# Kernel tuning notes

Measured on AMD Instinct MI355X. Metric: run time of the kernel, lower is better.

The kernel has to match this reference:

```python
import jax, jax.numpy as jnp
import numpy as np

# ---- config (matches init_kwargs) ----
B, C_IN, L, T = 32, 12, 1024, 64
C1, C2, K = 64, 128, 7
PAD = K // 2
NUM_CLASSES = 4
GAIN = 2.0
TH1, TH2 = 0.5, 0.5
TAU1, TAU2 = 1.0, 0.9
RESET = 0.0


def setup_inputs() -> dict:
    key = jax.random.key(0)
    ks = jax.random.split(key, 7)
    x = jax.random.normal(ks[0], (B, C_IN, L, T), dtype=jnp.float32)
    w1 = jax.random.normal(ks[1], (C1, C_IN, K), dtype=jnp.float32) * 0.1
    b1 = jax.random.normal(ks[2], (C1,), dtype=jnp.float32) * 0.01
    w2 = jax.random.normal(ks[3], (C2, C1, K), dtype=jnp.float32) * 0.05
    b2 = jax.random.normal(ks[4], (C2,), dtype=jnp.float32) * 0.01
    fc_w = jax.random.normal(ks[5], (NUM_CLASSES, C2), dtype=jnp.float32) * 0.1
    fc_b = jax.random.normal(ks[6], (NUM_CLASSES,), dtype=jnp.float32) * 0.01
    return {"x": x, "w1": w1, "b1": b1, "w2": w2, "b2": b2, "fc_w": fc_w, "fc_b": fc_b}


def _conv1d(x, w, b):
    # x: [B, Cin, L], w: [Cout, Cin, K] -> [B, Cout, L] (same padding)
    y = jax.lax.conv_general_dilated(
        x, w, window_strides=(1,), padding=[(PAD, PAD)],
        dimension_numbers=("NCW", "OIW", "NCW"))
    return y + b[None, :, None]


def _lif(v, inp, tau, thresh):
    # v <- v + (inp - v)/tau; spike = (v >= thresh); reset spiked neurons
    v = v + (inp - v) / tau
    spike = (v >= thresh).astype(inp.dtype)
    v = jnp.where(spike > 0, jnp.asarray(RESET, inp.dtype), v)
    return v, spike


def reference(x, w1, b1, w2, b2, fc_w, fc_b):
    # QuantStub/DeQuantStub are identity in the fp32 eager model.
    xs = jnp.transpose(x, (3, 0, 1, 2))  # [T, B, C_IN, L]

    def step(carry, xt):
        v1, v2, acc = carry
        h1 = _conv1d(xt, w1, b1) * GAIN
        v1, s1 = _lif(v1, h1, TAU1, TH1)
        h2 = _conv1d(s1, w2, b2) * GAIN
        v2, s2 = _lif(v2, h2, TAU2, TH2)
        return (v1, v2, acc + s2), None

    v1_0 = jnp.zeros((B, C1, L), x.dtype)
    v2_0 = jnp.zeros((B, C2, L), x.dtype)
    acc0 = jnp.zeros((B, C2, L), x.dtype)
    (_, _, acc), _ = jax.lax.scan(step, (v1_0, v2_0, acc0), xs)

    out = acc / jnp.asarray(T, x.dtype)          # [B, C2, L]
    out = jnp.mean(out, axis=-1)                  # AdaptiveAvgPool1d(1) + squeeze
    return out @ fc_w.T + fc_b                    # [B, NUM_CLASSES]
```

## Files before the change

### kernel.cpp

```cpp
#include <hip/hip_runtime.h>
#include <hip/hip_bf16.h>
#include <cstdint>

#define B_   32
#define CIN  12
#define L_   1024
#define T_   64
#define C1_  64
#define C2_  128
#define K_   7
#define PAD_ 3

typedef __attribute__((ext_vector_type(8))) short short8;
typedef __attribute__((ext_vector_type(4))) float float4v;

#define WS_S1T   0ull
#define WS_W2HI  268435456ull
#define WS_W1F   (WS_W2HI + 114688ull)
#define WS_POOL  (WS_W1F + 32768ull)
#define WS_ZP    (WS_POOL + 16384ull)

#define GLOAD_LDS(SRC, DST)                                                        \
    __builtin_amdgcn_global_load_lds(                                              \
        (const __attribute__((address_space(1))) unsigned int*)(const void*)(SRC), \
        (__attribute__((address_space(3))) unsigned int*)(void*)(DST), 16, 0, 0)

static __device__ __forceinline__ ushort bf16_hi(float f) {
    __hip_bfloat16 h = __float2bfloat16(f);
    ushort u; __builtin_memcpy(&u, &h, 2); return u;
}
static __device__ __forceinline__ float bf16_back(ushort u) {
    __hip_bfloat16 h; __builtin_memcpy(&h, &u, 2); return __bfloat162float(h);
}

__global__ __launch_bounds__(256) void k0_prep_w2(const float* __restrict__ w2,
                                                  ushort* __restrict__ w2hi,
                                                  float* __restrict__ pool,
                                                  ushort* __restrict__ zp) {
    int i = blockIdx.x * 256 + threadIdx.x;
    if (i < B_ * C2_) pool[i] = 0.0f;
    if (i < 2048) zp[i] = 0;
    if (i >= C2_ * K_ * C1_) return;
    int c2 = i / (K_ * C1_);
    int r_ = i % (K_ * C1_);
    int kk = r_ / C1_;
    int c1 = r_ % C1_;
    float w = w2[(c2 * C1_ + c1) * K_ + kk];
    ushort uh = bf16_hi(w);
    int h    = c1 >> 5;
    int c1r  = c1 & 31;
    int e    = c1r >> 4;
    int kq   = (c1r >> 2) & 3;
    int rr   = c1r & 3;
    int j    = e * 4 + rr;
    int mt   = c2 >> 4;
    int lane = kq * 16 + (c2 & 15);
    int o    = ((((kk * 2 + h) * 8 + mt) * 64) + lane) * 8 + j;
    w2hi[o] = uh;
}

__global__ __launch_bounds__(256) void k0_prep_w1(const float* __restrict__ w1,
                                                  ushort* __restrict__ w1f) {
    int i = blockIdx.x * 256 + threadIdx.x;
    if (i >= 16384) return;
    int j    = i & 7;
    int lane = (i >> 3) & 63;
    int mf   = (i >> 9) & 3;
    int ks   = (i >> 11) & 3;
    int cp   = i >> 13;
    int k    = ks * 32 + (lane >> 4) * 8 + j;
    int dl   = k >> 4;
    int slot = k & 15;
    int c1   = mf * 16 + (lane & 15);
    float v  = (slot < CIN && dl < K_) ? w1[(c1 * CIN + slot) * K_ + dl] : 0.0f;
    ushort hi = bf16_hi(v);
    float  rem = v - bf16_back(hi);
    ushort lo = bf16_hi(rem);
    w1f[i] = cp ? lo : hi;
}

__global__ __launch_bounds__(512, 4) void k1_conv1_mfma(const float* __restrict__ x,
                                                        const ushort* __restrict__ w1f,
                                                        const float* __restrict__ b1,
                                                        ushort* __restrict__ s1t) {
    __shared__ __align__(16) ushort S[14 * 2048];
    int tid  = threadIdx.x;
    int lane = tid & 63;
    int wl   = tid >> 6;
    int b    = blockIdx.y;
    int bx   = blockIdx.x;
    int swz  = ((bx & 7) << 4) | (bx >> 3);
    int lb   = swz * 8;

    #pragma unroll
    for (int it = 0; it < 4; ++it) {
        int u = it * 512 + tid;
        if (u < 1792) {
            int t  = u & 63;
            int h2 = (u >> 6) & 1;
            int lp = u >> 7;
            int gl = lb + lp - PAD_;
            bool ok = (gl >= 0) && (gl < L_);
            short8 hv, lv;
            #pragma unroll
            for (int jj = 0; jj < 8; ++jj) {
                int cin = h2 * 8 + jj;
                float v = (ok && cin < CIN)
                    ? x[(((size_t)b * CIN + cin) * L_ + gl) * T_ + t] : 0.0f;
                ushort hb = bf16_hi(v);
                ushort lo = bf16_hi(v - bf16_back(hb));
                hv[jj] = (short)hb;
                lv[jj] = (short)lo;
            }
            int nt = t >> 4, t15 = t & 15;
            int base = lp * 2048 + nt * 256 + h2 * 128 + t15 * 8;
            *(short8*)&S[base]        = hv;
            *(short8*)&S[base + 1024] = lv;
        }
    }
    __syncthreads();

    int t15 = lane & 15;
    int h2l = (lane >> 4) & 1;
    int kqh = lane >> 5;

    float4v acc[4][4];
    #pragma unroll
    for (int i = 0; i < 4; ++i)
        #pragma unroll
        for (int jn = 0; jn < 4; ++jn)
            acc[i][jn] = (float4v){0.0f, 0.0f, 0.0f, 0.0f};

    #pragma unroll
    for (int ks = 0; ks < 4; ++ks) {
        int dtap = ks * 2 + kqh;
        int lpr  = (dtap == 7) ? 0 : (wl + dtap);
        int rb   = lpr * 2048 + h2l * 128 + t15 * 8;
        short8 bh[4], bl[4];
        #pragma unroll
        for (int nt = 0; nt < 4; ++nt) {
            bh[nt] = *(const short8*)&S[rb + nt * 256];
            bl[nt] = *(const short8*)&S[rb + nt * 256 + 1024];
        }
        #pragma unroll
        for (int mf = 0; mf < 4; ++mf) {
            const ushort* ap = w1f + ((size_t)(ks * 4 + mf) * 64 + lane) * 8;
            short8 ah = *(const short8*)ap;
            short8 al = *(const short8*)(ap + 8192);
            #pragma unroll
            for (int nt = 0; nt < 4; ++nt) {
                acc[mf][nt] = __builtin_amdgcn_mfma_f32_16x16x32_bf16(ah, bh[nt], acc[mf][nt], 0, 0, 0);
                acc[mf][nt] = __builtin_amdgcn_mfma_f32_16x16x32_bf16(al, bh[nt], acc[mf][nt], 0, 0, 0);
                acc[mf][nt] = __builtin_amdgcn_mfma_f32_16x16x32_bf16(ah, bl[nt], acc[mf][nt], 0, 0, 0);
            }
        }
    }

    int l  = lb + wl;
    int kq = lane >> 4;
    #pragma unroll
    for (int h = 0; h < 2; ++h) {
        float4v be0 = *(const float4v*)&b1[h * 32 + kq * 4];
        float4v be1 = *(const float4v*)&b1[h * 32 + 16 + kq * 4];
        #pragma unroll
        for (int nt = 0; nt < 4; ++nt) {
            uint s0 = (acc[2 * h][nt][0] + be0[0] >= 0.25f) ? 0x3F80u : 0u;
            uint s1 = (acc[2 * h][nt][1] + be0[1] >= 0.25f) ? 0x3F80u : 0u;
            uint s2 = (acc[2 * h][nt][2] + be0[2] >= 0.25f) ? 0x3F80u : 0u;
            uint s3 = (acc[2 * h][nt][3] + be0[3] >= 0.25f) ? 0x3F80u : 0u;
            uint s4 = (acc[2 * h + 1][nt][0] + be1[0] >= 0.25f) ? 0x3F80u : 0u;
            uint s5 = (acc[2 * h + 1][nt][1] + be1[1] >= 0.25f) ? 0x3F80u : 0u;
            uint s6 = (acc[2 * h + 1][nt][2] + be1[2] >= 0.25f) ? 0x3F80u : 0u;
            uint s7 = (acc[2 * h + 1][nt][3] + be1[3] >= 0.25f) ? 0x3F80u : 0u;
            uint4 u4 = { s0 | (s1 << 16), s2 | (s3 << 16),
                         s4 | (s5 << 16), s6 | (s7 << 16) };
            size_t off = ((((size_t)b * L_ + l) * 2 + h) * T_ + (nt * 16 + t15)) * 32 + kq * 8;
            *(uint4*)&s1t[off] = u4;
        }
    }
}

__global__ __launch_bounds__(512, 2) void k2_conv2_lif(const ushort* __restrict__ s1t,
                                                       const ushort* __restrict__ w2hi,
                                                       const float* __restrict__ b2,
                                                       float* __restrict__ pool,
                                                       const ushort* __restrict__ zp) {
    __shared__ __align__(16) unsigned char lds_raw[40960];
    ushort* S = (ushort*)lds_raw;
    int tid    = threadIdx.x;
    int wv     = tid >> 6;
    int lane   = tid & 63;
    int wn     = wv >> 1;
    int wm     = wv & 1;
    int b      = blockIdx.y;
    int bx     = blockIdx.x;
    int swz    = ((bx & 7) << 5) | (bx >> 3);
    int lb     = swz * 4;
    int lane15 = lane & 15;
    int kq     = lane >> 4;
    int srcoff = lane15 * 32 + (lane >> 4) * 8;

    float4v acc[4][4];
    #pragma unroll
    for (int i = 0; i < 4; ++i)
        #pragma unroll
        for (int j = 0; j < 4; ++j)
            acc[i][j] = (float4v){0.0f, 0.0f, 0.0f, 0.0f};

    #pragma unroll 1
    for (int h = 0; h < 2; ++h) {
        __syncthreads();
        #pragma unroll
        for (int r0 = 0; r0 < 2; ++r0) {
            int r = r0 * 8 + wv;
            if (r < 10) {
                int gl = lb + r - PAD_;
                const ushort* srow = (gl >= 0 && gl < L_)
                    ? &s1t[(((size_t)b * L_ + gl) * 2 + h) * 2048] : zp;
                const ushort* s = srow + srcoff;
                ushort* d = &S[r * 2048];
                GLOAD_LDS(s,        d);
                GLOAD_LDS(s + 512,  d + 512);
                GLOAD_LDS(s + 1024, d + 1024);
                GLOAD_LDS(s + 1536, d + 1536);
            }
        }
        __syncthreads();
        #pragma unroll 2
        for (int kk = 0; kk < K_; ++kk) {
            int lp = wn + kk;
            short8 bf[4];
            #pragma unroll
            for (int nt = 0; nt < 4; ++nt)
                bf[nt] = *(const short8*)&S[lp * 2048 + nt * 512 + lane * 8];
            #pragma unroll
            for (int mf = 0; mf < 4; ++mf) {
                int aoff = (((kk * 2 + h) * 8 + wm * 4 + mf) * 64 + lane) * 8;
                short8 ahi = *(const short8*)&w2hi[aoff];
                #pragma unroll
                for (int nt = 0; nt < 4; ++nt)
                    acc[mf][nt] = __builtin_amdgcn_mfma_f32_16x16x32_bf16(ahi, bf[nt], acc[mf][nt], 0, 0, 0);
            }
        }
    }
    __syncthreads();

    float* E = ((float*)lds_raw) + wv * 1088;
    int c2v = wm * 64 + lane;
    const float Af = 1.0f - 1.0f / 0.9f;
    const float Cs = 2.0f / 0.9f;
    float D = b2[c2v] * Cs;
    float v = 0.0f;
    uint cnt = 0u;
    #pragma unroll
    for (int nt = 0; nt < 4; ++nt) {
        *(float4v*)&E[lane15 * 68 + 0 * 16 + kq * 4] = acc[0][nt];
        *(float4v*)&E[lane15 * 68 + 1 * 16 + kq * 4] = acc[1][nt];
        *(float4v*)&E[lane15 * 68 + 2 * 16 + kq * 4] = acc[2][nt];
        *(float4v*)&E[lane15 * 68 + 3 * 16 + kq * 4] = acc[3][nt];
        __builtin_amdgcn_s_waitcnt(0);
        #pragma unroll
        for (int tt = 0; tt < 16; ++tt) {
            float e = fmaf(E[tt * 68 + lane], Cs, D);
            v = fmaf(Af, v, e);
            bool sp = (v >= 0.5f);
            cnt += sp ? 1u : 0u;
            v = sp ? 0.0f : v;
        }
        __builtin_amdgcn_s_waitcnt(0);
    }
    atomicAdd(&pool[b * C2_ + c2v], (float)cnt);
}

__global__ __launch_bounds__(128) void k3_fc(const float* __restrict__ pool,
                                             const float* __restrict__ fcw,
                                             const float* __restrict__ fcb,
                                             float* __restrict__ out) {
    int i = threadIdx.x;
    int b = i >> 2, c = i & 3;
    float o = fcb[c];
    #pragma unroll 8
    for (int c2 = 0; c2 < C2_; ++c2)
        o = fmaf(fcw[c * C2_ + c2], pool[b * C2_ + c2] * (1.0f / 65536.0f), o);
    out[b * 4 + c] = o;
}

extern "C" void kernel_launch(void* const* d_in, const int* in_sizes, int n_in,
                              void* d_out, int out_size, void* d_ws, size_t ws_size,
                              hipStream_t stream) {
    const float* x   = (const float*)d_in[0];
    const float* w1  = (const float*)d_in[1];
    const float* b1  = (const float*)d_in[2];
    const float* w2  = (const float*)d_in[3];
    const float* b2  = (const float*)d_in[4];
    const float* fcw = (const float*)d_in[5];
    const float* fcb = (const float*)d_in[6];
    float* out = (float*)d_out;

    char* ws = (char*)d_ws;
    ushort* s1t  = (ushort*)(ws + WS_S1T);
    ushort* w2h  = (ushort*)(ws + WS_W2HI);
    ushort* w1f  = (ushort*)(ws + WS_W1F);
    float*  pool = (float*)(ws + WS_POOL);
    ushort* zp   = (ushort*)(ws + WS_ZP);

    k0_prep_w2<<<dim3((C2_ * K_ * C1_ + 255) / 256), dim3(256), 0, stream>>>(w2, w2h, pool, zp);
    k0_prep_w1<<<dim3(64), dim3(256), 0, stream>>>(w1, w1f);
    k1_conv1_mfma<<<dim3(L_ / 8, B_), dim3(512), 0, stream>>>(x, w1f, b1, s1t);
    k2_conv2_lif<<<dim3(L_ / 4, B_), dim3(512), 0, stream>>>(s1t, w2h, b2, pool, zp);
    k3_fc<<<dim3(1), dim3(128), 0, stream>>>(pool, fcw, fcb, out);
}
```

Before: 553.6 us.

## Double-buffer conv2 input loads and shrink conv1 block tile

In the conv2 kernel, the loads for both halves of the channel dimension are now issued up front into two LDS buffers (80 KB of dynamic shared memory), and it waits only on the first half before computing, so the second half's loads overlap the first half's MFMA work. The conv1 kernel moves to 256-thread blocks covering 4 positions instead of 8, which doubles the grid and cuts its LDS use. The larger LDS footprint in conv2 can lower occupancy, and smaller conv1 tiles reload more halo input.

```diff
diff --git a/kernel.cpp b/kernel.cpp
--- a/kernel.cpp
+++ b/kernel.cpp
@@ -79,44 +79,42 @@
     w1f[i] = cp ? lo : hi;
 }
 
-__global__ __launch_bounds__(512, 4) void k1_conv1_mfma(const float* __restrict__ x,
+__global__ __launch_bounds__(256, 2) void k1_conv1_mfma(const float* __restrict__ x,
                                                         const ushort* __restrict__ w1f,
                                                         const float* __restrict__ b1,
                                                         ushort* __restrict__ s1t) {
-    __shared__ __align__(16) ushort S[14 * 2048];
+    __shared__ __align__(16) ushort S[10 * 2048];
     int tid  = threadIdx.x;
     int lane = tid & 63;
     int wl   = tid >> 6;
     int b    = blockIdx.y;
     int bx   = blockIdx.x;
-    int swz  = ((bx & 7) << 4) | (bx >> 3);
-    int lb   = swz * 8;
-
-    #pragma unroll
-    for (int it = 0; it < 4; ++it) {
-        int u = it * 512 + tid;
-        if (u < 1792) {
-            int t  = u & 63;
-            int h2 = (u >> 6) & 1;
-            int lp = u >> 7;
-            int gl = lb + lp - PAD_;
-            bool ok = (gl >= 0) && (gl < L_);
-            short8 hv, lv;
-            #pragma unroll
-            for (int jj = 0; jj < 8; ++jj) {
-                int cin = h2 * 8 + jj;
-                float v = (ok && cin < CIN)
-                    ? x[(((size_t)b * CIN + cin) * L_ + gl) * T_ + t] : 0.0f;
-                ushort hb = bf16_hi(v);
-                ushort lo = bf16_hi(v - bf16_back(hb));
-                hv[jj] = (short)hb;
-                lv[jj] = (short)lo;
-            }
-            int nt = t >> 4, t15 = t & 15;
-            int base = lp * 2048 + nt * 256 + h2 * 128 + t15 * 8;
-            *(short8*)&S[base]        = hv;
-            *(short8*)&S[base + 1024] = lv;
-        }
+    int swz  = ((bx & 7) << 5) | (bx >> 3);
+    int lb   = swz * 4;
+
+    #pragma unroll
+    for (int it = 0; it < 5; ++it) {
+        int u  = it * 256 + tid;
+        int t  = u & 63;
+        int h2 = (u >> 6) & 1;
+        int lp = u >> 7;
+        int gl = lb + lp - PAD_;
+        bool ok = (gl >= 0) && (gl < L_);
+        short8 hv, lv;
+        #pragma unroll
+        for (int jj = 0; jj < 8; ++jj) {
+            int cin = h2 * 8 + jj;
+            float v = (ok && cin < CIN)
+                ? x[(((size_t)b * CIN + cin) * L_ + gl) * T_ + t] : 0.0f;
+            ushort hb = bf16_hi(v);
+            ushort lo = bf16_hi(v - bf16_back(hb));
+            hv[jj] = (short)hb;
+            lv[jj] = (short)lo;
+        }
+        int nt = t >> 4, t15 = t & 15;
+        int base = lp * 2048 + nt * 256 + h2 * 128 + t15 * 8;
+        *(short8*)&S[base]        = hv;
+        *(short8*)&S[base + 1024] = lv;
     }
     __syncthreads();
 
@@ -180,13 +178,42 @@
     }
 }
 
+#define K2_ISSUE(BUF, H) do {                                                     \
+    _Pragma("unroll")                                                             \
+    for (int i_ = 0; i_ < 5; ++i_) {                                              \
+        int q_ = wv * 5 + i_;                                                     \
+        int r_ = q_ >> 2, c_ = q_ & 3;                                            \
+        int gl_ = lb + r_ - PAD_;                                                 \
+        const ushort* srow_ = (gl_ >= 0 && gl_ < L_)                              \
+            ? &s1t[(((size_t)b * L_ + gl_) * 2 + (H)) * 2048] : zp;               \
+        GLOAD_LDS(srow_ + c_ * 512 + srcoff, Sb + (BUF) * 20480 + r_ * 2048 + c_ * 512); \
+    } } while (0)
+
+#define K2_COMPUTE(BUF, H) do {                                                   \
+    _Pragma("unroll 2")                                                           \
+    for (int kk = 0; kk < K_; ++kk) {                                             \
+        int lp = wn + kk;                                                         \
+        short8 bf[4];                                                             \
+        _Pragma("unroll")                                                         \
+        for (int nt = 0; nt < 4; ++nt)   \
+            bf[nt] = *(const short8*)&Sb[(BUF) * 20480 + lp * 2048 + nt * 512 + lane * 8]; \
+        _Pragma("unroll")                                                         \
+        for (int mf = 0; mf < 4; ++mf) {                                          \
+            int aoff = (((kk * 2 + (H)) * 8 + wm * 4 + mf) * 64 + lane) * 8;      \
+            short8 ahi = *(const short8*)&w2hi[aoff];                             \
+            _Pragma("unroll")                                                     \
+            for (int nt = 0; nt < 4; ++nt)                                        \
+                acc[mf][nt] = __builtin_amdgcn_mfma_f32_16x16x32_bf16(ahi, bf[nt], acc[mf][nt], 0, 0, 0); \
+        }                                                                         \
+    } } while (0)
+
 __global__ __launch_bounds__(512, 2) void k2_conv2_lif(const ushort* __restrict__ s1t,
                                                        const ushort* __restrict__ w2hi,
                                                        const float* __restrict__ b2,
                                                        float* __restrict__ pool,
                                                        const ushort* __restrict__ zp) {
-    __shared__ __align__(16) unsigned char lds_raw[40960];
-    ushort* S = (ushort*)lds_raw;
+    extern __shared__ __align__(16) unsigned char lds_raw[];
+    ushort* Sb = (ushort*)lds_raw;
     int tid    = threadIdx.x;
     int wv     = tid >> 6;
     int lane   = tid & 63;
@@ -207,43 +234,14 @@
         for (int j = 0; j < 4; ++j)
             acc[i][j] = (float4v){0.0f, 0.0f, 0.0f, 0.0f};
 
-    #pragma unroll 1
-    for (int h = 0; h < 2; ++h) {
-        __syncthreads();
-        #pragma unroll
-        for (int r0 = 0; r0 < 2; ++r0) {
-            int r = r0 * 8 + wv;
-            if (r < 10) {
-                int gl = lb + r - PAD_;
-                const ushort* srow = (gl >= 0 && gl < L_)
-                    ? &s1t[(((size_t)b * L_ + gl) * 2 + h) * 2048] : zp;
-                const ushort* s = srow + srcoff;
-                ushort* d = &S[r * 2048];
-                GLOAD_LDS(s,        d);
-                GLOAD_LDS(s + 512,  d + 512);
-                GLOAD_LDS(s + 1024, d + 1024);
-                GLOAD_LDS(s + 1536, d + 1536);
-            }
-        }
-        __syncthreads();
-        #pragma unroll 2
-        for (int kk = 0; kk < K_; ++kk) {
-            int lp = wn + kk;
-            short8 bf[4];
-            #pragma unroll
-            for (int nt = 0; nt < 4; ++nt)
-                bf[nt] = *(const short8*)&S[lp * 2048 + nt * 512 + lane * 8];
-            #pragma unroll
-            for (int mf = 0; mf < 4; ++mf) {
-                int aoff = (((kk * 2 + h) * 8 + wm * 4 + mf) * 64 + lane) * 8;
-                short8 ahi = *(const short8*)&w2hi[aoff];
-                #pragma unroll
-                for (int nt = 0; nt < 4; ++nt)
-                    acc[mf][nt] = __builtin_amdgcn_mfma_f32_16x16x32_bf16(ahi, bf[nt], acc[mf][nt], 0, 0, 0);
-            }
-        }
-    }
-    __syncthreads();
+    K2_ISSUE(0, 0);
+    K2_ISSUE(1, 1);
+    asm volatile("s_waitcnt vmcnt(5)" ::: "memory");
+    __builtin_amdgcn_s_barrier();
+    K2_COMPUTE(0, 0);
+    asm volatile("s_waitcnt vmcnt(0)" ::: "memory");
+    __builtin_amdgcn_s_barrier();
+    K2_COMPUTE(1, 1);
 
     float* E = ((float*)lds_raw) + wv * 1088;
     int c2v = wm * 64 + lane;
@@ -306,7 +304,7 @@
 
     k0_prep_w2<<<dim3((C2_ * K_ * C1_ + 255) / 256), dim3(256), 0, stream>>>(w2, w2h, pool, zp);
     k0_prep_w1<<<dim3(64), dim3(256), 0, stream>>>(w1, w1f);
-    k1_conv1_mfma<<<dim3(L_ / 8, B_), dim3(512), 0, stream>>>(x, w1f, b1, s1t);
-    k2_conv2_lif<<<dim3(L_ / 4, B_), dim3(512), 0, stream>>>(s1t, w2h, b2, pool, zp);
+    k1_conv1_mfma<<<dim3(L_ / 4, B_), dim3(256), 0, stream>>>(x, w1f, b1, s1t);
+    k2_conv2_lif<<<dim3(L_ / 4, B_), dim3(512), 81920, stream>>>(s1t, w2h, b2, pool, zp);
     k3_fc<<<dim3(1), dim3(128), 0, stream>>>(pool, fcw, fcb, out);
 }
```

Measured after the change: 547.9 us. Within noise of the previous version (-1.0%).
